# Kernel tuning notes

Measured on AMD Instinct MI355X. Metric: run time of the kernel, lower is better.

Reference implementation:

```python
import jax, jax.numpy as jnp
import numpy as np

B, S, H = 4, 4096, 4096
E, G, TOPK_GROUP, TOP_K = 160, 8, 3, 6
SCALE = 16.0      # routed_scaling_factor (norm_topk_prob=False)
ALPHA = 0.001     # aux_loss_alpha
M = 3             # config.M for communication aux loss


def setup_inputs() -> dict:
    key = jax.random.key(0)
    k1, k2 = jax.random.split(key)
    hidden_states = jax.random.normal(k1, (B, S, H), dtype=jnp.float32)
    # kaiming_uniform_(a=sqrt(5)) on (E, H): bound = 1/sqrt(fan_in)
    bound = 1.0 / np.sqrt(H)
    weight = jax.random.uniform(k2, (E, H), minval=-bound, maxval=bound, dtype=jnp.float32)
    return {"hidden_states": hidden_states, "weight": weight}


def _gate(hidden_states, weight):
    b, s, h = hidden_states.shape
    x = hidden_states.reshape(-1, h).astype(jnp.float32)          # [T, H]
    logits = x @ weight.astype(jnp.float32).T                      # [T, E]
    scores = jax.nn.softmax(logits, axis=-1)
    T = b * s
    # group-limited greedy top-k
    group_scores = scores.reshape(T, G, E // G).max(axis=-1)       # [T, G]
    _, group_idx = jax.lax.top_k(group_scores, TOPK_GROUP)         # [T, topk_group]
    group_mask = jnp.zeros((T, G), scores.dtype).at[
        jnp.arange(T)[:, None], group_idx].set(1.0)                # [T, G]
    score_mask = jnp.repeat(group_mask, E // G, axis=1)            # [T, E]
    tmp_scores = jnp.where(score_mask > 0, scores, 0.0)
    topk_weight, topk_idx = jax.lax.top_k(tmp_scores, TOP_K)       # [T, k]
    topk_weight = topk_weight * SCALE
    # --- aux losses (training, seq_aux=True, alpha>0) ---
    idx_flat = topk_idx.reshape(b, s * TOP_K)                      # [b, s*k]
    counts = jax.vmap(
        lambda idx: jnp.zeros((E,), jnp.float32).at[idx].add(1.0)
    )(idx_flat)                                                    # [b, E]
    ce = counts / (s * TOP_K / E)
    mean_scores = scores.reshape(b, s, E).mean(axis=1)             # [b, E]
    aux_expert = (ce * mean_scores).sum(axis=1).mean() * ALPHA
    ce_g = ce.reshape(b, G, -1).mean(axis=-1)                      # [b, G]
    ms_g = mean_scores.reshape(b, G, -1).mean(axis=-1)             # [b, G]
    aux_device = (ce_g * ms_g).sum(axis=1).mean() * ALPHA
    ce2 = counts.reshape(b, G, -1).sum(axis=-1) / (M * s / G)      # [b, G]
    aux_comm = (ce2 * ms_g).sum(axis=1).mean() * ALPHA
    aux_loss = aux_expert + aux_device + aux_comm
    return topk_idx, topk_weight, aux_loss


def reference(hidden_states, weight):
    return _gate(hidden_states, weight)
```

## Files before the change

### kernel.cpp

```cpp
#include <hip/hip_runtime.h>

typedef _Float16 half8 __attribute__((ext_vector_type(8)));
typedef float f32x4 __attribute__((ext_vector_type(4)));

#define H    4096
#define NE   160
#define BM   64
#define TPB  1024
#define NIT  64


__global__ __launch_bounds__(256) void prep_kernel(
    const float* __restrict__ w, _Float16* __restrict__ Wf)
{
    int F    = blockIdx.x * 256 + threadIdx.x;
    int lane = F & 63;
    int t10  = (F >> 6) % 10;
    int ks   = F / 640;
    int e    = t10 * 16 + (lane & 15);
    int k0   = ks * 32 + (lane >> 4) * 8;
    const float* p = w + (size_t)e * H + k0;
    float4 v0 = *(const float4*)p;
    float4 v1 = *(const float4*)(p + 4);
    float vv[8] = {v0.x, v0.y, v0.z, v0.w, v1.x, v1.y, v1.z, v1.w};
    half8 h0, h1;
#pragma unroll
    for (int j = 0; j < 8; ++j) {
        float s = vv[j] * 64.f;
        _Float16 a = (_Float16)s;
        h0[j] = a;
        h1[j] = (_Float16)((s - (float)a) * 2048.f);
    }
    half8* out = (half8*)Wf;
    out[(ks * 20 + t10) * 64 + lane]      = h0;
    out[(ks * 20 + 10 + t10) * 64 + lane] = h1;
}

#define GLOAD_LDS(SRC, DST)                                                    \
    __builtin_amdgcn_global_load_lds(                                          \
        (const __attribute__((address_space(1))) unsigned int*)(SRC),          \
        (__attribute__((address_space(3))) unsigned int*)(DST), 16, 0, 0)

#define STAGE_W(ITN, WOFF)                                                     \
    do {                                                                       \
        const _Float16* _s = Wf + ((size_t)(ITN) * 2560 + tid) * 8;            \
        GLOAD_LDS(_s,            s_w + (WOFF) + (size_t)tid * 8);              \
        GLOAD_LDS(_s + 8192,     s_w + (WOFF) + (size_t)(tid + 1024) * 8);     \
        if (tid < 512)                                                         \
            GLOAD_LDS(_s + 16384, s_w + (WOFF) + (size_t)(tid + 2048) * 8);    \
    } while (0)

#define STAGE_X(ITN, XOFF)                                                     \
    do {                                                                       \
        int _row = tid >> 4, _ch = tid & 15;                                   \
        const float* _s = x + (size_t)(row0 + _row) * H + (ITN) * 64           \
                          + ((_ch ^ (_row & 7)) << 2);                         \
        GLOAD_LDS(_s, s_x + (XOFF) + tid * 4);                                 \
    } while (0)

#define CONVERT(U0, U1)                                                        \
    do {                                                                       \
        float v0=U0.x, v1=U0.y, v2=U0.z, v3=U0.w;                              \
        float v4=U1.x, v5=U1.y, v6=U1.z, v7=U1.w;                              \
        _Float16 h;                                                            \
        h=(_Float16)v0; a0[0]=h; a1[0]=(_Float16)((v0-(float)h)*2048.f);       \
        h=(_Float16)v1; a0[1]=h; a1[1]=(_Float16)((v1-(float)h)*2048.f);       \
        h=(_Float16)v2; a0[2]=h; a1[2]=(_Float16)((v2-(float)h)*2048.f);       \
        h=(_Float16)v3; a0[3]=h; a1[3]=(_Float16)((v3-(float)h)*2048.f);       \
        h=(_Float16)v4; a0[4]=h; a1[4]=(_Float16)((v4-(float)h)*2048.f);       \
        h=(_Float16)v5; a0[5]=h; a1[5]=(_Float16)((v5-(float)h)*2048.f);       \
        h=(_Float16)v6; a0[6]=h; a1[6]=(_Float16)((v6-(float)h)*2048.f);       \
        h=(_Float16)v7; a0[7]=h; a1[7]=(_Float16)((v7-(float)h)*2048.f);       \
    } while (0)

#define COMPUTE(WOFF, XOFF)                                                    \
    do {                                                                       \
        const float* _xr = s_x + (XOFF) + arow * 64;                           \
        float4 u0 = *(const float4*)(_xr + ((ch0 ^ r7) << 2));                 \
        float4 u1 = *(const float4*)(_xr + ((ch1 ^ r7) << 2));                 \
        const half8* B = (const half8*)(s_w + (WOFF)) + sbase;                 \
        half8 b0[5], b1[5];                                                    \
        _Pragma("unroll")                                                      \
        for (int _t = 0; _t < 5; ++_t) {                                       \
            b0[_t] = B[_t * 64];                                               \
            b1[_t] = B[640 + _t * 64];                                         \
        }                                                                      \
        half8 a0, a1;                                                          \
        CONVERT(u0, u1);                                                       \
        _Pragma("unroll")                                                      \
        for (int _t = 0; _t < 5; ++_t) {                                       \
            accH[_t] = __builtin_amdgcn_mfma_f32_16x16x32_f16(a0, b0[_t], accH[_t], 0, 0, 0); \
            accL[_t] = __builtin_amdgcn_mfma_f32_16x16x32_f16(a1, b0[_t], accL[_t], 0, 0, 0); \
            accL[_t] = __builtin_amdgcn_mfma_f32_16x16x32_f16(a0, b1[_t], accL[_t], 0, 0, 0); \
        }                                                                      \
    } while (0)

__global__ __launch_bounds__(TPB) void gate_kernel(
    const float* __restrict__ x, const _Float16* __restrict__ Wf,
    float* __restrict__ outIdx, float* __restrict__ outW,
    float* __restrict__ gcnt, float* __restrict__ gssum)
{
    __shared__ __align__(16) _Float16 s_w[2 * 2560 * 8];
    __shared__ __align__(16) float    s_x[2 * 4096];
    __shared__ float s_mx[BM], s_inv[BM];
    __shared__ int   s_cnt[NE];
    float* s_log = (float*)s_w;

    const int tid  = threadIdx.x;
    const int lane = tid & 63;
    const int wv   = tid >> 6;
    const int kh   = wv >> 3;
    const int mh   = (wv >> 1) & 3;
    const int nh   = wv & 1;
    const int row0 = blockIdx.x * BM;

    if (tid < NE) s_cnt[tid] = 0;

    f32x4 accH[5], accL[5];
#pragma unroll
    for (int t = 0; t < 5; ++t) { accH[t] = (f32x4){0,0,0,0}; accL[t] = (f32x4){0,0,0,0}; }

    const int sbase = kh * 1280 + nh * 320 + lane;
    const int arow  = mh * 16 + (lane & 15);
    const int r7    = arow & 7;
    const int ch0   = kh * 8 + (lane >> 4) * 2;
    const int ch1   = ch0 + 1;

    STAGE_W(0, 0);
    STAGE_X(0, 0);
    __syncthreads();

    for (int it = 0; it < NIT; it += 2) {
        if (it + 1 < NIT) { STAGE_W(it + 1, 20480); STAGE_X(it + 1, 4096); }
        COMPUTE(0, 0);
        __syncthreads();

        if (it + 2 < NIT) { STAGE_W(it + 2, 0); STAGE_X(it + 2, 0); }
        COMPUTE(20480, 4096);
        __syncthreads();
    }

    const int crow  = mh * 16 + (lane >> 4) * 4;
    const int ccol0 = nh * 80 + (lane & 15);
    if (kh == 0) {
#pragma unroll
        for (int t = 0; t < 5; ++t)
#pragma unroll
            for (int r = 0; r < 4; ++r)
                s_log[(crow + r) * 161 + ccol0 + t * 16] =
                    (accH[t][r] + accL[t][r] * (1.0f / 2048.f)) * (1.0f / 64.f);
    }
    __syncthreads();
    if (kh == 1) {
#pragma unroll
        for (int t = 0; t < 5; ++t)
#pragma unroll
            for (int r = 0; r < 4; ++r)
                s_log[(crow + r) * 161 + ccol0 + t * 16] +=
                    (accH[t][r] + accL[t][r] * (1.0f / 2048.f)) * (1.0f / 64.f);
    }
    __syncthreads();

    if (tid < BM) {
        const float* L = &s_log[tid * 161];
        float gmax[8];
        float mx = -3.4e38f;
#pragma unroll
        for (int g = 0; g < 8; ++g) {
            float m = L[g * 20];
            for (int j = 1; j < 20; ++j) m = fmaxf(m, L[g * 20 + j]);
            gmax[g] = m;
            mx = fmaxf(mx, m);
        }
        float sum = 0.f;
        for (int e = 0; e < NE; ++e) sum += __expf(L[e] - mx);
        float inv = 1.0f / sum;
        s_mx[tid]  = mx;
        s_inv[tid] = inv;

        unsigned sel = 0;
        float pv = 3.4e38f; int pi = -1;
        for (int it = 0; it < 3; ++it) {
            float bv = -3.4e38f; int bi = 0;
            for (int g = 0; g < 8; ++g) {
                float v = gmax[g];
                bool below = (v < pv) || (v == pv && g > pi);
                if (below && v > bv) { bv = v; bi = g; }
            }
            sel |= 1u << bi;
            pv = bv; pi = bi;
        }

        const int tok = row0 + tid;
        float pv2 = 3.4e38f; int pi2 = -1;
        for (int it = 0; it < 6; ++it) {
            float bv = -3.4e38f; int bi = 0;
            for (int g = 0; g < 8; ++g) {
                if (!((sel >> g) & 1u)) continue;
                for (int j = 0; j < 20; ++j) {
                    int e = g * 20 + j;
                    float v = L[e];
                    bool below = (v < pv2) || (v == pv2 && e > pi2);
                    if (below && v > bv) { bv = v; bi = e; }
                }
            }
            pv2 = bv; pi2 = bi;
            outIdx[(size_t)tok * 6 + it] = (float)bi;
            outW[(size_t)tok * 6 + it]   = __expf(bv - mx) * inv * 16.0f;
            atomicAdd(&s_cnt[bi], 1);
        }
    }
    __syncthreads();

    if (tid < NE) {
        float ss = 0.f;
        for (int t2 = 0; t2 < BM; ++t2)
            ss += __expf(s_log[t2 * 161 + tid] - s_mx[t2]) * s_inv[t2];
        const int b = row0 >> 12;
        atomicAdd(&gssum[b * NE + tid], ss);
        atomicAdd(&gcnt[b * NE + tid], (float)s_cnt[tid]);
    }
}

__global__ __launch_bounds__(64) void aux_kernel(
    const float* __restrict__ gcnt, const float* __restrict__ gssum,
    float* __restrict__ out)
{
    const int lane = threadIdx.x;
    float part = 0.f;
    if (lane < 32) {
        const int b = lane >> 3, g = lane & 7;
        const float* cn = gcnt  + b * NE + g * 20;
        const float* sm = gssum + b * NE + g * 20;
        float s1 = 0.f, sc = 0.f, sms = 0.f;
        for (int j = 0; j < 20; ++j) {
            float ce = cn[j] * (1.0f / 153.6f);
            float ms = sm[j] * (1.0f / 4096.0f);
            s1  += ce * ms;
            sc  += cn[j];
            sms += ms;
        }
        float ceg = sc * (1.0f / 153.6f) * (1.0f / 20.0f);
        float msg = sms * (1.0f / 20.0f);
        float ce2 = sc * (1.0f / 1536.0f);
        part = s1 + ceg * msg + ce2 * msg;
    }
#pragma unroll
    for (int off = 32; off > 0; off >>= 1) part += __shfl_down(part, off);
    if (lane == 0) out[0] = part * (0.001f * 0.25f);
}

extern "C" void kernel_launch(void* const* d_in, const int* in_sizes, int n_in,
                              void* d_out, int out_size, void* d_ws, size_t ws_size,
                              hipStream_t stream)
{
    (void)in_sizes; (void)n_in; (void)out_size; (void)ws_size;
    const float* x = (const float*)d_in[0];
    const float* w = (const float*)d_in[1];
    float* out = (float*)d_out;

    _Float16* Wf  = (_Float16*)d_ws;
    float* gcnt  = (float*)(Wf + (size_t)NE * H * 2);
    float* gssum = gcnt + 4 * NE;

    hipMemsetAsync(gcnt, 0, 2 * 4 * NE * sizeof(float), stream);

    prep_kernel<<<(NE * H / 8) / 256, 256, 0, stream>>>(w, Wf);
    gate_kernel<<<16384 / BM, TPB, 0, stream>>>(
        x, Wf, out, out + 98304, gcnt, gssum);
    aux_kernel<<<1, 64, 0, stream>>>(gcnt, gssum, out + 196608);
}
```

Before: 195.5 us.

## Stage activations in 256-column single-buffered blocks instead of per-iteration double buffers

Activation tiles are now loaded into LDS as one 64x256 block covering four K-iterations, with four async global-to-LDS loads per thread. Before, a 64x64 tile was double-buffered every iteration. The aim is longer contiguous row reads and fewer X staging events, while the weight tiles keep their double buffer. In exchange the X load is no longer overlapped with compute: an extra barrier at each block boundary exposes its latency. LDS use for X also doubles.

```diff
diff --git a/kernel.cpp b/kernel.cpp
--- a/kernel.cpp
+++ b/kernel.cpp
@@ -50,12 +50,16 @@
             GLOAD_LDS(_s + 16384, s_w + (WOFF) + (size_t)(tid + 2048) * 8);    \
     } while (0)
 
-#define STAGE_X(ITN, XOFF)                                                     \
-    do {                                                                       \
-        int _row = tid >> 4, _ch = tid & 15;                                   \
-        const float* _s = x + (size_t)(row0 + _row) * H + (ITN) * 64           \
-                          + ((_ch ^ (_row & 7)) << 2);                         \
-        GLOAD_LDS(_s, s_x + (XOFF) + tid * 4);                                 \
+#define STAGE_X8(T8)                                                           \
+    do {                                                                       \
+        _Pragma("unroll")                                                      \
+        for (int _rd = 0; _rd < 4; ++_rd) {                                    \
+            int _ii  = _rd * 1024 + tid;                                       \
+            int _row = _ii >> 6, _c = _ii & 63;                                \
+            const float* _s = x + (size_t)(row0 + _row) * H + (T8) * 256       \
+                              + ((_c ^ (_row & 7)) << 2);                      \
+            GLOAD_LDS(_s, s_x + _ii * 4);                                      \
+        }                                                                      \
     } while (0)
 
 #define CONVERT(U0, U1)                                                        \
@@ -73,11 +77,12 @@
         h=(_Float16)v7; a0[7]=h; a1[7]=(_Float16)((v7-(float)h)*2048.f);       \
     } while (0)
 
-#define COMPUTE(WOFF, XOFF)                                                    \
-    do {                                                                       \
-        const float* _xr = s_x + (XOFF) + arow * 64;                           \
-        float4 u0 = *(const float4*)(_xr + ((ch0 ^ r7) << 2));                 \
-        float4 u1 = *(const float4*)(_xr + ((ch1 ^ r7) << 2));                 \
+#define COMPUTE(WOFF, P)                                                       \
+    do {                                                                       \
+        const int _j0 = ((P) * 2 + kh) * 8 + q2;                               \
+        const float* _xr = s_x + arow * 256;                                   \
+        float4 u0 = *(const float4*)(_xr + ((_j0 ^ r7) << 2));                 \
+        float4 u1 = *(const float4*)(_xr + (((_j0 + 1) ^ r7) << 2));           \
         const half8* B = (const half8*)(s_w + (WOFF)) + sbase;                 \
         half8 b0[5], b1[5];                                                    \
         _Pragma("unroll")                                                      \
@@ -101,7 +106,7 @@
     float* __restrict__ gcnt, float* __restrict__ gssum)
 {
     __shared__ __align__(16) _Float16 s_w[2 * 2560 * 8];
-    __shared__ __align__(16) float    s_x[2 * 4096];
+    __shared__ __align__(16) float    s_x[64 * 256];
     __shared__ float s_mx[BM], s_inv[BM];
     __shared__ int   s_cnt[NE];
     float* s_log = (float*)s_w;
@@ -123,20 +128,26 @@
     const int sbase = kh * 1280 + nh * 320 + lane;
     const int arow  = mh * 16 + (lane & 15);
     const int r7    = arow & 7;
-    const int ch0   = kh * 8 + (lane >> 4) * 2;
-    const int ch1   = ch0 + 1;
-
+    const int q2    = (lane >> 4) * 2;
+
+    STAGE_X8(0);
     STAGE_W(0, 0);
-    STAGE_X(0, 0);
-    __syncthreads();
-
-    for (int it = 0; it < NIT; it += 2) {
-        if (it + 1 < NIT) { STAGE_W(it + 1, 20480); STAGE_X(it + 1, 4096); }
+    __syncthreads();
+
+    for (int b = 0; b < NIT; b += 4) {
+        if (b) { STAGE_X8(b >> 2); }
+        STAGE_W(b + 1, 20480);
+        if (b) __syncthreads();
         COMPUTE(0, 0);
         __syncthreads();
-
-        if (it + 2 < NIT) { STAGE_W(it + 2, 0); STAGE_X(it + 2, 0); }
-        COMPUTE(20480, 4096);
+        STAGE_W(b + 2, 0);
+        COMPUTE(20480, 1);
+        __syncthreads();
+        STAGE_W(b + 3, 20480);
+        COMPUTE(0, 2);
+        __syncthreads();
+        if (b + 4 < NIT) STAGE_W(b + 4, 0);
+        COMPUTE(20480, 3);
         __syncthreads();
     }
 
```

Result: slower. 199.8 us (+2.2%).
